# Kernel optimization log

Hardware: AMD Instinct MI355X
Metric: run time of the kernel (lower is better)

The kernel has to match this reference:

```python
import jax, jax.numpy as jnp
import numpy as np
from jax import lax

B, C, H, W = 8, 256, 64, 64
E, K, OUT = 9, 3, 256
EPS = 1e-5


def setup_inputs() -> dict:
    key = jax.random.key(0)
    ks = jax.random.split(key, 12)
    return {
        "x": jax.random.normal(ks[0], (B, C, H, W), jnp.float32),
        "w_experts": jax.random.normal(ks[1], (E, C, K, K), jnp.float32) * 0.1,  # depthwise kernels (O=C, I=1 folded)
        "bn_gamma": jax.random.normal(ks[2], (E, C), jnp.float32) * 0.1 + 1.0,
        "bn_beta": jax.random.normal(ks[3], (E, C), jnp.float32) * 0.1,
        "bn_mean": jax.random.normal(ks[4], (E, C), jnp.float32) * 0.1,
        "bn_var": jax.random.uniform(ks[5], (E, C), jnp.float32, 0.5, 1.5),
        "scales": jnp.full((E, C), 0.1, jnp.float32),
        "w_out": jax.random.normal(ks[6], (OUT, C), jnp.float32) * (1.0 / np.sqrt(C)),  # 1x1 conv weight
        "out_gamma": jax.random.normal(ks[7], (OUT,), jnp.float32) * 0.1 + 1.0,
        "out_beta": jax.random.normal(ks[8], (OUT,), jnp.float32) * 0.1,
        "out_mean": jax.random.normal(ks[9], (OUT,), jnp.float32) * 0.1,
        "out_var": jax.random.uniform(ks[10], (OUT,), jnp.float32, 0.5, 1.5),
    }


def reference(x, w_experts, bn_gamma, bn_beta, bn_mean, bn_var, scales,
              w_out, out_gamma, out_beta, out_mean, out_var):
    # All E depthwise convs in ONE grouped conv: groups=C, E outputs per group.
    # kernel (E,C,K,K) -> (C,E,K,K) -> (C*E, 1, K, K); output group c holds experts of channel c.
    k = jnp.transpose(w_experts, (1, 0, 2, 3)).reshape(C * E, 1, K, K)
    y = lax.conv_general_dilated(
        x, k, window_strides=(1, 1), padding="SAME",
        feature_group_count=C,
        dimension_numbers=("NCHW", "OIHW", "NCHW"),
    )  # [B, C*E, H, W]
    y = y.reshape(x.shape[0], C, E, H, W)

    # Fold BN (eval-mode, running stats) and per-expert channel scale, then sum over experts.
    t = bn_gamma * lax.rsqrt(bn_var + EPS)          # [E, C]
    eff_scale = t * scales                          # [E, C]
    eff_bias = ((bn_beta - bn_mean * t) * scales).sum(0)  # [C]
    moe = jnp.einsum("bcehw,ec->bchw", y, eff_scale) + eff_bias[None, :, None, None]
    moe = jax.nn.silu(moe)

    # out_prj: 1x1 conv + BN + SiLU
    out = jnp.einsum("bchw,oc->bohw", moe, w_out)
    t2 = out_gamma * lax.rsqrt(out_var + EPS)       # [OUT]
    out = out * t2[None, :, None, None] + (out_beta - out_mean * t2)[None, :, None, None]
    return jax.nn.silu(out)
```

## Files before the change

kernel.cpp:

```cpp
#include <hip/hip_runtime.h>

#define EPS 1e-5f

typedef __attribute__((ext_vector_type(8))) __bf16 bf16x8;
typedef __attribute__((ext_vector_type(4))) float f32x4;

__device__ __forceinline__ float silu_f(float v) {
  return v / (1.f + __expf(-v));
}

__global__ __launch_bounds__(256) void prep_kernel(
    const float* __restrict__ w_experts, const float* __restrict__ bn_gamma,
    const float* __restrict__ bn_beta, const float* __restrict__ bn_mean,
    const float* __restrict__ bn_var, const float* __restrict__ scales,
    const float* __restrict__ w_out, const float* __restrict__ out_gamma,
    const float* __restrict__ out_beta, const float* __restrict__ out_mean,
    const float* __restrict__ out_var,
    float* __restrict__ eff_kernel, float* __restrict__ eff_bias,
    __bf16* __restrict__ w_eff, float* __restrict__ bias2)
{
  const int t = threadIdx.x;
  if (blockIdx.x == 0) {
    const int c = t;
    float k9[9];
#pragma unroll
    for (int r = 0; r < 9; ++r) k9[r] = 0.f;
    float bias = 0.f;
    for (int e = 0; e < 9; ++e) {
      const int ec = e * 256 + c;
      const float tt = bn_gamma[ec] * rsqrtf(bn_var[ec] + EPS);
      const float sc = scales[ec];
      const float es = tt * sc;
      bias += (bn_beta[ec] - bn_mean[ec] * tt) * sc;
      const float* wp = w_experts + (size_t)ec * 9;
#pragma unroll
      for (int r = 0; r < 9; ++r) k9[r] += es * wp[r];
    }
#pragma unroll
    for (int r = 0; r < 9; ++r) eff_kernel[c * 9 + r] = k9[r];
    eff_bias[c] = bias;
    const float t2 = out_gamma[c] * rsqrtf(out_var[c] + EPS);
    bias2[c] = out_beta[c] - out_mean[c] * t2;
  } else {
    const int i = (blockIdx.x - 1) * 256 + t;
    const int o = i >> 8;
    const float t2 = out_gamma[o] * rsqrtf(out_var[o] + EPS);
    w_eff[i] = (__bf16)(w_out[i] * t2);
  }
}

__global__ __launch_bounds__(512, 4) void fused_kernel(
    const float* __restrict__ x, const float* __restrict__ eff_kernel,
    const float* __restrict__ eff_bias, const __bf16* __restrict__ w_eff,
    const float* __restrict__ bias2, float* __restrict__ out)
{
  __shared__ __align__(16) __bf16 B_lds[64 * 264];
  __shared__ float kern_s[256 * 9];
  __shared__ float bias_s[256];
  const int t = threadIdx.x;
  const int id = blockIdx.x;
  const int b = id & 7;
  const int h = id >> 3;

  for (int i = t; i < 2304; i += 512) kern_s[i] = eff_kernel[i];
  if (t < 256) bias_s[t] = eff_bias[t];
  __syncthreads();

  const int lane = t & 63;
  const int wv = t >> 6;
  const int lg = lane >> 4;
  const int wq = lane & 15;
  const int w4 = wq * 4;
  const bool up_ok = (h > 0), dn_ok = (h < 63);

#pragma unroll
  for (int cg = 0; cg < 2; ++cg) {
#pragma unroll
    for (int cc4 = 0; cc4 < 4; ++cc4) {
      const int ch = cg * 128 + wv * 16 + cc4 * 4 + lg;
      const float* xc = x + (size_t)(b * 256 + ch) * 4096;

      float4 v0, v1, v2;
      v1 = *(const float4*)(xc + h * 64 + w4);
      if (up_ok) v0 = *(const float4*)(xc + (h - 1) * 64 + w4);
      else       v0 = make_float4(0.f, 0.f, 0.f, 0.f);
      if (dn_ok) v2 = *(const float4*)(xc + (h + 1) * 64 + w4);
      else       v2 = make_float4(0.f, 0.f, 0.f, 0.f);

      float k[9];
#pragma unroll
      for (int j = 0; j < 9; ++j) k[j] = kern_s[ch * 9 + j];
      const float bias = bias_s[ch];

      float rowv[3][6];
      const float4 vv[3] = {v0, v1, v2};
#pragma unroll
      for (int r = 0; r < 3; ++r) {
        float vl = __shfl_up(vv[r].w, 1);
        float vr = __shfl_down(vv[r].x, 1);
        rowv[r][0] = (wq == 0) ? 0.f : vl;
        rowv[r][1] = vv[r].x;
        rowv[r][2] = vv[r].y;
        rowv[r][3] = vv[r].z;
        rowv[r][4] = vv[r].w;
        rowv[r][5] = (wq == 15) ? 0.f : vr;
      }

#pragma unroll
      for (int j = 0; j < 4; ++j) {
        float s = bias;
#pragma unroll
        for (int r = 0; r < 3; ++r)
          s += k[r * 3] * rowv[r][j] + k[r * 3 + 1] * rowv[r][j + 1] + k[r * 3 + 2] * rowv[r][j + 2];
        B_lds[(w4 + j) * 264 + ch] = (__bf16)silu_f(s);
      }
    }
  }
  __syncthreads();

  const int quad = lg, l15 = wq;
  const int wave_o = wv * 32;

  f32x4 acc[2][4];
#pragma unroll
  for (int i = 0; i < 2; ++i)
#pragma unroll
    for (int j = 0; j < 4; ++j) acc[i][j] = (f32x4){0.f, 0.f, 0.f, 0.f};

#pragma unroll
  for (int kk = 0; kk < 8; ++kk) {
    bf16x8 af[2], bf[4];
#pragma unroll
    for (int i = 0; i < 2; ++i)
      af[i] = *(const bf16x8*)&w_eff[(size_t)(wave_o + i * 16 + l15) * 256 + kk * 32 + quad * 8];
#pragma unroll
    for (int j = 0; j < 4; ++j)
      bf[j] = *(const bf16x8*)&B_lds[(j * 16 + l15) * 264 + kk * 32 + quad * 8];
#pragma unroll
    for (int i = 0; i < 2; ++i)
#pragma unroll
      for (int j = 0; j < 4; ++j)
        acc[i][j] = __builtin_amdgcn_mfma_f32_16x16x32_bf16(af[i], bf[j], acc[i][j], 0, 0, 0);
  }

  float* outb = out + (size_t)b * 256 * 4096 + h * 64;
#pragma unroll
  for (int i = 0; i < 2; ++i) {
#pragma unroll
    for (int r = 0; r < 4; ++r) {
      const int o = wave_o + i * 16 + quad * 4 + r;
      const float bo = bias2[o];
#pragma unroll
      for (int j = 0; j < 4; ++j) {
        const int p = j * 16 + l15;
        outb[(size_t)o * 4096 + p] = silu_f(acc[i][j][r] + bo);
      }
    }
  }
}

extern "C" void kernel_launch(void* const* d_in, const int* in_sizes, int n_in,
                              void* d_out, int out_size, void* d_ws, size_t ws_size,
                              hipStream_t stream) {
  const float* x         = (const float*)d_in[0];
  const float* w_experts = (const float*)d_in[1];
  const float* bn_gamma  = (const float*)d_in[2];
  const float* bn_beta   = (const float*)d_in[3];
  const float* bn_mean   = (const float*)d_in[4];
  const float* bn_var    = (const float*)d_in[5];
  const float* scales    = (const float*)d_in[6];
  const float* w_out     = (const float*)d_in[7];
  const float* out_gamma = (const float*)d_in[8];
  const float* out_beta  = (const float*)d_in[9];
  const float* out_mean  = (const float*)d_in[10];
  const float* out_var   = (const float*)d_in[11];
  float* out = (float*)d_out;

  char* ws = (char*)d_ws;
  float* eff_kernel = (float*)(ws);
  float* eff_bias   = (float*)(ws + 9216);
  __bf16* w_eff     = (__bf16*)(ws + 10240);
  float* bias2      = (float*)(ws + 141312);

  hipLaunchKernelGGL(prep_kernel, dim3(257), dim3(256), 0, stream,
                     w_experts, bn_gamma, bn_beta, bn_mean, bn_var, scales,
                     w_out, out_gamma, out_beta, out_mean, out_var,
                     eff_kernel, eff_bias, w_eff, bias2);
  hipLaunchKernelGGL(fused_kernel, dim3(512), dim3(512), 0, stream,
                     x, eff_kernel, eff_bias, w_eff, bias2, out);
}
```

Measured before the change: 124.5 us.

## Split each output row across two blocks to double grid parallelism

Each block now handles half an image row (32 pixels) instead of a full row, so the grid doubles to 1024 blocks. The LDS tile shrinks to a padded stride of 258, and launch bounds are raised to allow 8 blocks per CU. Depthwise halo values are now fetched with scalar global loads instead of warp shuffles. The aim is better latency hiding and load balance across CUs. The cost is that each block re-reads the full 1x1 weight matrix while doing half as much MFMA work. The 258 stride also leaves the 16-byte LDS vector reads misaligned.

```diff
diff --git a/kernel.cpp b/kernel.cpp
--- a/kernel.cpp
+++ b/kernel.cpp
@@ -49,18 +49,21 @@
   }
 }
 
-__global__ __launch_bounds__(512, 4) void fused_kernel(
+#define BSTRIDE 258
+__global__ __launch_bounds__(512, 8) void fused_kernel(
     const float* __restrict__ x, const float* __restrict__ eff_kernel,
     const float* __restrict__ eff_bias, const __bf16* __restrict__ w_eff,
     const float* __restrict__ bias2, float* __restrict__ out)
 {
-  __shared__ __align__(16) __bf16 B_lds[64 * 264];
+  __shared__ __align__(16) __bf16 B_lds[32 * BSTRIDE];
   __shared__ float kern_s[256 * 9];
   __shared__ float bias_s[256];
   const int t = threadIdx.x;
   const int id = blockIdx.x;
   const int b = id & 7;
-  const int h = id >> 3;
+  const int rest = id >> 3;
+  const int h = rest >> 1;
+  const int half = rest & 1;
 
   for (int i = t; i < 2304; i += 512) kern_s[i] = eff_kernel[i];
   if (t < 256) bias_s[t] = eff_bias[t];
@@ -68,82 +71,76 @@
 
   const int lane = t & 63;
   const int wv = t >> 6;
-  const int lg = lane >> 4;
-  const int wq = lane & 15;
-  const int w4 = wq * 4;
+  const int chl = lane >> 3;
+  const int pxl = lane & 7;
+  const int w0 = half * 32 + pxl * 4;
   const bool up_ok = (h > 0), dn_ok = (h < 63);
+  const bool left_ok = (w0 > 0), right_ok = (w0 + 4 < 64);
 
 #pragma unroll
-  for (int cg = 0; cg < 2; ++cg) {
+  for (int it = 0; it < 4; ++it) {
+    const int ch = it * 64 + wv * 8 + chl;
+    const float* xc = x + (size_t)(b * 256 + ch) * 4096;
+
+    float rowv[3][6];
 #pragma unroll
-    for (int cc4 = 0; cc4 < 4; ++cc4) {
-      const int ch = cg * 128 + wv * 16 + cc4 * 4 + lg;
-      const float* xc = x + (size_t)(b * 256 + ch) * 4096;
+    for (int r = 0; r < 3; ++r) {
+      const int hh = h + r - 1;
+      if ((r == 0 && !up_ok) || (r == 2 && !dn_ok)) {
+#pragma unroll
+        for (int q = 0; q < 6; ++q) rowv[r][q] = 0.f;
+      } else {
+        const float* xr = xc + hh * 64;
+        const float4 m = *(const float4*)(xr + w0);
+        rowv[r][0] = left_ok ? xr[w0 - 1] : 0.f;
+        rowv[r][1] = m.x;  rowv[r][2] = m.y;
+        rowv[r][3] = m.z;  rowv[r][4] = m.w;
+        rowv[r][5] = right_ok ? xr[w0 + 4] : 0.f;
+      }
+    }
 
-      float4 v0, v1, v2;
-      v1 = *(const float4*)(xc + h * 64 + w4);
-      if (up_ok) v0 = *(const float4*)(xc + (h - 1) * 64 + w4);
-      else       v0 = make_float4(0.f, 0.f, 0.f, 0.f);
-      if (dn_ok) v2 = *(const float4*)(xc + (h + 1) * 64 + w4);
-      else       v2 = make_float4(0.f, 0.f, 0.f, 0.f);
-
-      float k[9];
+    float k[9];
 #pragma unroll
-      for (int j = 0; j < 9; ++j) k[j] = kern_s[ch * 9 + j];
-      const float bias = bias_s[ch];
-
-      float rowv[3][6];
-      const float4 vv[3] = {v0, v1, v2};
-#pragma unroll
-      for (int r = 0; r < 3; ++r) {
-        float vl = __shfl_up(vv[r].w, 1);
-        float vr = __shfl_down(vv[r].x, 1);
-        rowv[r][0] = (wq == 0) ? 0.f : vl;
-        rowv[r][1] = vv[r].x;
-        rowv[r][2] = vv[r].y;
-        rowv[r][3] = vv[r].z;
-        rowv[r][4] = vv[r].w;
-        rowv[r][5] = (wq == 15) ? 0.f : vr;
-      }
+    for (int j = 0; j < 9; ++j) k[j] = kern_s[ch * 9 + j];
+    const float bias = bias_s[ch];
 
 #pragma unroll
-      for (int j = 0; j < 4; ++j) {
-        float s = bias;
+    for (int j = 0; j < 4; ++j) {
+      float s = bias;
 #pragma unroll
-        for (int r = 0; r < 3; ++r)
-          s += k[r * 3] * rowv[r][j] + k[r * 3 + 1] * rowv[r][j + 1] + k[r * 3 + 2] * rowv[r][j + 2];
-        B_lds[(w4 + j) * 264 + ch] = (__bf16)silu_f(s);
-      }
+      for (int r = 0; r < 3; ++r)
+        s += k[r * 3] * rowv[r][j] + k[r * 3 + 1] * rowv[r][j + 1] + k[r * 3 + 2] * rowv[r][j + 2];
+      B_lds[(pxl * 4 + j) * BSTRIDE + ch] = (__bf16)silu_f(s);
     }
   }
   __syncthreads();
 
-  const int quad = lg, l15 = wq;
+  const int quad = lane >> 4, l15 = lane & 15;
   const int wave_o = wv * 32;
 
-  f32x4 acc[2][4];
+  f32x4 acc[2][2];
 #pragma unroll
   for (int i = 0; i < 2; ++i)
 #pragma unroll
-    for (int j = 0; j < 4; ++j) acc[i][j] = (f32x4){0.f, 0.f, 0.f, 0.f};
+    for (int j = 0; j < 2; ++j) acc[i][j] = (f32x4){0.f, 0.f, 0.f, 0.f};
 
 #pragma unroll
   for (int kk = 0; kk < 8; ++kk) {
-    bf16x8 af[2], bf[4];
+    bf16x8 af[2], bf[2];
 #pragma unroll
     for (int i = 0; i < 2; ++i)
       af[i] = *(const bf16x8*)&w_eff[(size_t)(wave_o + i * 16 + l15) * 256 + kk * 32 + quad * 8];
 #pragma unroll
-    for (int j = 0; j < 4; ++j)
-      bf[j] = *(const bf16x8*)&B_lds[(j * 16 + l15) * 264 + kk * 32 + quad * 8];
+    for (int j = 0; j < 2; ++j)
+      bf[j] = *(const bf16x8*)&B_lds[(j * 16 + l15) * BSTRIDE + kk * 32 + quad * 8];
 #pragma unroll
     for (int i = 0; i < 2; ++i)
 #pragma unroll
-      for (int j = 0; j < 4; ++j)
+      for (int j = 0; j < 2; ++j)
         acc[i][j] = __builtin_amdgcn_mfma_f32_16x16x32_bf16(af[i], bf[j], acc[i][j], 0, 0, 0);
   }
 
-  float* outb = out + (size_t)b * 256 * 4096 + h * 64;
+  float* outb = out + (size_t)b * 256 * 4096 + h * 64 + half * 32;
 #pragma unroll
   for (int i = 0; i < 2; ++i) {
 #pragma unroll
@@ -151,7 +148,7 @@
       const int o = wave_o + i * 16 + quad * 4 + r;
       const float bo = bias2[o];
 #pragma unroll
-      for (int j = 0; j < 4; ++j) {
+      for (int j = 0; j < 2; ++j) {
         const int p = j * 16 + l15;
         outb[(size_t)o * 4096 + p] = silu_f(acc[i][j][r] + bo);
       }
@@ -186,6 +183,6 @@
                      w_experts, bn_gamma, bn_beta, bn_mean, bn_var, scales,
                      w_out, out_gamma, out_beta, out_mean, out_var,
                      eff_kernel, eff_bias, w_eff, bias2);
-  hipLaunchKernelGGL(fused_kernel, dim3(512), dim3(512), 0, stream,
+  hipLaunchKernelGGL(fused_kernel, dim3(1024), dim3(512), 0, stream,
                      x, eff_kernel, eff_bias, w_eff, bias2, out);
 }
```

After: 134.9 us. +8.3%, slower.
